# Performance work log

Hardware: AMD Instinct MI355X
Metric: run time of the kernel (lower is better)

Reference implementation:

```python
import jax, jax.numpy as jnp
import numpy as np

EPS_BN = 1e-3  # nn.BatchNorm1d(num_channels, eps=0.001)
B, C, N = 16, 256, 2048
NUM_SA = 4


def _bn(x, g, b, m, v):
    # eval-mode BatchNorm1d over channel dim of [B, C, N]
    return g[:, None] * (x - m[:, None]) * jax.lax.rsqrt(v[:, None] + EPS_BN) + b[:, None]


def _sa_layer(x, qk_w, v_w, v_b, t_w, t_b, g, b, m, var):
    # q_conv and k_conv share weights -> energy = (Wx)^T (Wx)
    q = jnp.einsum('oc,bcn->bon', qk_w, x)              # [B, C//4, N]
    energy = jnp.einsum('bcm,bcn->bmn', q, q)           # [B, N, N]
    attn = jax.nn.softmax(energy, axis=-1)
    # offset-attention: extra column-sum normalization (dim=1)
    attn = attn / (1e-9 + attn.sum(axis=1, keepdims=True))
    xv = jnp.einsum('oc,bcn->bon', v_w, x) + v_b[:, None]   # [B, C, N]
    x_r = jnp.einsum('bcn,bnm->bcm', xv, attn)              # bmm(x_v, attention)
    t = jnp.einsum('oc,bcn->bon', t_w, x - x_r) + t_b[:, None]
    return x + jax.nn.relu(_bn(t, g, b, m, var))


def setup_inputs() -> dict:
    key = jax.random.key(0)
    ks = jax.random.split(key, 24)
    f32 = jnp.float32
    d = {}
    d['x'] = jax.random.normal(ks[0], (B, C, N), dtype=f32)
    d['conv1_w'] = jax.random.normal(ks[1], (C, C), dtype=f32) * 0.05
    d['conv2_w'] = jax.random.normal(ks[2], (C, C), dtype=f32) * 0.05
    for i, nm in enumerate(['bn1', 'bn2']):
        kk = jax.random.split(ks[3 + i], 4)
        d[nm + '_g'] = 1.0 + 0.05 * jax.random.normal(kk[0], (C,), dtype=f32)
        d[nm + '_b'] = 0.05 * jax.random.normal(kk[1], (C,), dtype=f32)
        d[nm + '_m'] = 0.05 * jax.random.normal(kk[2], (C,), dtype=f32)
        d[nm + '_v'] = jax.random.uniform(kk[3], (C,), dtype=f32, minval=0.5, maxval=1.5)
    d['sa_qk_w'] = jax.random.normal(ks[5], (NUM_SA, C // 4, C), dtype=f32) * 0.05
    d['sa_v_w'] = jax.random.normal(ks[6], (NUM_SA, C, C), dtype=f32) * 0.05
    d['sa_v_b'] = jax.random.normal(ks[7], (NUM_SA, C), dtype=f32) * 0.05
    d['sa_t_w'] = jax.random.normal(ks[8], (NUM_SA, C, C), dtype=f32) * 0.05
    d['sa_t_b'] = jax.random.normal(ks[9], (NUM_SA, C), dtype=f32) * 0.05
    d['sa_g'] = 1.0 + 0.05 * jax.random.normal(ks[10], (NUM_SA, C), dtype=f32)
    d['sa_b'] = 0.05 * jax.random.normal(ks[11], (NUM_SA, C), dtype=f32)
    d['sa_m'] = 0.05 * jax.random.normal(ks[12], (NUM_SA, C), dtype=f32)
    d['sa_var'] = jax.random.uniform(ks[13], (NUM_SA, C), dtype=f32, minval=0.5, maxval=1.5)
    d['flag'] = 0  # False -> primary bn branch
    return d


def reference(x, conv1_w, conv2_w, bn1_g, bn1_b, bn1_m, bn1_v,
              bn2_g, bn2_b, bn2_m, bn2_v,
              sa_qk_w, sa_v_w, sa_v_b, sa_t_w, sa_t_b,
              sa_g, sa_b, sa_m, sa_var, flag):
    h = jax.nn.relu(_bn(jnp.einsum('oc,bcn->bon', conv1_w, x), bn1_g, bn1_b, bn1_m, bn1_v))
    h = jax.nn.relu(_bn(jnp.einsum('oc,bcn->bon', conv2_w, h), bn2_g, bn2_b, bn2_m, bn2_v))
    outs = []
    for i in range(NUM_SA):
        h = _sa_layer(h, sa_qk_w[i], sa_v_w[i], sa_v_b[i], sa_t_w[i], sa_t_b[i],
                      sa_g[i], sa_b[i], sa_m[i], sa_var[i])
        outs.append(h)
    return jnp.concatenate(outs, axis=1)  # [B, 4*C, N]
```

## Files before the change

kernel.cpp:

```cpp
#include <hip/hip_runtime.h>
#include <hip/hip_bf16.h>
#include <hip/hip_fp16.h>

static constexpr int Bn = 16;
static constexpr int Cc = 256;
static constexpr int Nn = 2048;
static constexpr int C4 = 64;
static constexpr float LOG2E = 1.4426950408889634f;

typedef _Float16 half_t;
typedef __attribute__((ext_vector_type(8))) _Float16 half8;
typedef __attribute__((ext_vector_type(4))) _Float16 half4;
typedef __attribute__((ext_vector_type(8))) short short8;
typedef __attribute__((ext_vector_type(4))) float float4v;

static constexpr long sNC = (long)Nn * Cc;
static constexpr long sNQ = (long)Nn * C4;

#define DEVI __device__ __forceinline__

DEVI float bf2f(unsigned short u) { return __uint_as_float(((unsigned)u) << 16); }
DEVI unsigned short f2bf(float f) {
    unsigned x = __float_as_uint(f);
    x += 0x7fffu + ((x >> 16) & 1u);
    return (unsigned short)(x >> 16);
}

DEVI void gload16(const void* g, void* l) {
    __builtin_amdgcn_global_load_lds(
        (const __attribute__((address_space(1))) unsigned int*)g,
        (__attribute__((address_space(3))) unsigned int*)l, 16, 0, 0);
}

enum { EPI_RAW = 0, EPI_H = 1, EPI_XV = 2 };

template<int MODE, int BM, int BN, int WI, int WJ, bool BF16OUT>
__global__ __launch_bounds__(WI * WJ * 64)
void mgemm(const half_t* __restrict__ A, long aB,
           const half_t* __restrict__ Bm, long bB,
           void* __restrict__ Yv, long yB, int ldy,
           const float* __restrict__ bias,
           const float* __restrict__ bng, const float* __restrict__ bnb,
           const float* __restrict__ bnm, const float* __restrict__ bnv,
           int K)
{
    constexpr int NW = WI * WJ;
    __shared__ __align__(16) half_t Als[2][BM][32];
    __shared__ __align__(16) half_t Bls[2][BN][32];

    const int tid  = threadIdx.x;
    const int w    = tid >> 6;
    const int lane = tid & 63;
    const int wi   = w % WI;
    const int wj   = w / WI;
    const int quad = lane >> 4, m16 = lane & 15;
    const int lr   = lane >> 2, lc = lane & 3;
    const int b    = blockIdx.z;
    const int j0   = blockIdx.x * BN;
    const int i0   = blockIdx.y * BM;

    const half_t* Ab = A + (size_t)b * aB;
    const half_t* Bb = Bm + (size_t)b * bB;

    float4v acc[4][4];
    #pragma unroll
    for (int i = 0; i < 4; ++i)
        #pragma unroll
        for (int j = 0; j < 4; ++j) acc[i][j] = (float4v)0.f;

    for (int k0 = 0; k0 < K; k0 += 64) {
        #pragma unroll
        for (int s = 0; s < 2; ++s) {
            const int kk = k0 + s * 32 + lc * 8;
            #pragma unroll
            for (int t = 0; t < BM / (16 * NW); ++t) {
                const int row = (t * NW + w) * 16;
                gload16(Ab + (size_t)(i0 + row + lr) * K + kk, &Als[s][row][0]);
            }
            #pragma unroll
            for (int t = 0; t < BN / (16 * NW); ++t) {
                const int row = (t * NW + w) * 16;
                gload16(Bb + (size_t)(j0 + row + lr) * K + kk, &Bls[s][row][0]);
            }
        }
        __syncthreads();
        #pragma unroll
        for (int s = 0; s < 2; ++s) {
            half8 af[4], bf[4];
            #pragma unroll
            for (int t = 0; t < 4; ++t)
                af[t] = *(const half8*)&Als[s][wi * 64 + t * 16 + m16][quad * 8];
            #pragma unroll
            for (int t = 0; t < 4; ++t)
                bf[t] = *(const half8*)&Bls[s][wj * 64 + t * 16 + m16][quad * 8];
            #pragma unroll
            for (int ti = 0; ti < 4; ++ti)
                #pragma unroll
                for (int tj = 0; tj < 4; ++tj)
                    acc[ti][tj] = __builtin_amdgcn_mfma_f32_16x16x32_f16(
                        af[ti], bf[tj], acc[ti][tj], 0, 0, 0);
        }
        __syncthreads();
    }

    #pragma unroll
    for (int ti = 0; ti < 4; ++ti) {
        const int il = i0 + wi * 64 + ti * 16 + quad * 4;
        #pragma unroll
        for (int tj = 0; tj < 4; ++tj) {
            const int jl = j0 + wj * 64 + tj * 16 + m16;
            float4v v = acc[ti][tj];
            if (MODE == EPI_RAW) {
                half4 o;
                #pragma unroll
                for (int r = 0; r < 4; ++r) o[r] = (half_t)v[r];
                *(half4*)((half_t*)Yv + (size_t)b * yB + (size_t)jl * ldy + il) = o;
            } else if (MODE == EPI_H) {
                half4 o;
                #pragma unroll
                for (int r = 0; r < 4; ++r) {
                    const float sc = bng[il + r] * rsqrtf(bnv[il + r] + 1e-3f);
                    const float sh = bnb[il + r] - bnm[il + r] * sc;
                    o[r] = (half_t)fmaxf(fmaf(v[r], sc, sh), 0.f);
                }
                *(half4*)((half_t*)Yv + (size_t)b * yB + (size_t)jl * ldy + il) = o;
            } else {
                const float bj = bias[jl];
                if (BF16OUT) {
                    ushort4 o;
                    o.x = f2bf(v[0] + bj); o.y = f2bf(v[1] + bj);
                    o.z = f2bf(v[2] + bj); o.w = f2bf(v[3] + bj);
                    *(ushort4*)((unsigned short*)Yv + (size_t)b * yB + (size_t)jl * ldy + il) = o;
                } else {
                    half4 o;
                    #pragma unroll
                    for (int r = 0; r < 4; ++r) o[r] = (half_t)(v[r] + bj);
                    *(half4*)((half_t*)Yv + (size_t)b * yB + (size_t)jl * ldy + il) = o;
                }
            }
        }
    }
}

__global__ __launch_bounds__(256)
void estats(const half_t* __restrict__ q, float* __restrict__ Pbuf)
{
    __shared__ __align__(16) half_t sA[128 * 64];
    __shared__ __align__(16) half_t sB[128 * 64];
    __shared__ float red[2][2][4][16][2];
    const int tid = threadIdx.x, w = tid >> 6, lane = tid & 63;
    const int wi = w & 1, wj = w >> 1, quad = lane >> 4, m16 = lane & 15;
    const int b = blockIdx.z, j0 = blockIdx.x * 128, i0 = blockIdx.y * 128;
    const half_t* qb = q + (size_t)b * sNQ;

    #pragma unroll
    for (int t = 0; t < 4; ++t) {
        const int g = w * 256 + t * 64 + lane;
        const int r = g >> 3, c = g & 7;
        const int cs = c ^ (r & 7);
        gload16(qb + (size_t)(i0 + r) * 64 + cs * 8, sA + (w * 256 + t * 64) * 8);
        gload16(qb + (size_t)(j0 + r) * 64 + cs * 8, sB + (w * 256 + t * 64) * 8);
    }
    __syncthreads();

    half8 an[4][2], bm[4][2];
    #pragma unroll
    for (int t = 0; t < 4; ++t)
        #pragma unroll
        for (int ks = 0; ks < 2; ++ks) {
            const int pc = ((ks * 4 + quad) ^ (m16 & 7)) * 8;
            an[t][ks] = *(const half8*)&sA[(wi * 64 + t * 16 + m16) * 64 + pc];
            bm[t][ks] = *(const half8*)&sB[(wj * 64 + t * 16 + m16) * 64 + pc];
        }

    #pragma unroll
    for (int tj = 0; tj < 4; ++tj) {
        float4v e[4];
        #pragma unroll
        for (int ti = 0; ti < 4; ++ti) {
            e[ti] = (float4v)0.f;
            e[ti] = __builtin_amdgcn_mfma_f32_16x16x32_f16(an[ti][0], bm[tj][0], e[ti], 0, 0, 0);
            e[ti] = __builtin_amdgcn_mfma_f32_16x16x32_f16(an[ti][1], bm[tj][1], e[ti], 0, 0, 0);
        }
        float lmax = -1e30f;
        #pragma unroll
        for (int ti = 0; ti < 4; ++ti)
            #pragma unroll
            for (int r = 0; r < 4; ++r) lmax = fmaxf(lmax, e[ti][r]);
        lmax = fmaxf(lmax, __shfl_xor(lmax, 16));
        lmax = fmaxf(lmax, __shfl_xor(lmax, 32));
        float ls = 0.f;
        #pragma unroll
        for (int ti = 0; ti < 4; ++ti)
            #pragma unroll
            for (int r = 0; r < 4; ++r) ls += __expf(e[ti][r] - lmax);
        ls += __shfl_xor(ls, 16);
        ls += __shfl_xor(ls, 32);
        if (quad == 0) { red[wi][wj][tj][m16][0] = lmax; red[wi][wj][tj][m16][1] = ls; }
    }
    __syncthreads();
    if (tid < 128) {
        const int wj2 = tid >> 6, tj2 = (tid >> 4) & 3, mm = tid & 15;
        const float m0 = red[0][wj2][tj2][mm][0], s0 = red[0][wj2][tj2][mm][1];
        const float m1 = red[1][wj2][tj2][mm][0], s1 = red[1][wj2][tj2][mm][1];
        const float M = fmaxf(m0, m1);
        const float S = s0 * __expf(m0 - M) + s1 * __expf(m1 - M);
        const int m = j0 + wj2 * 64 + tj2 * 16 + mm;
        *(float2*)(Pbuf + (((size_t)b * Nn + m) * 16 + blockIdx.y) * 2) = make_float2(M, S);
    }
}

__global__ __launch_bounds__(512)
void flashxr(const half_t* __restrict__ q, const half_t* __restrict__ xv,
             const half_t* __restrict__ h, const float* __restrict__ Pbuf,
             const half_t* __restrict__ tw, const float* __restrict__ tb,
             const float* __restrict__ bng, const float* __restrict__ bnb,
             const float* __restrict__ bnm, const float* __restrict__ bnv,
             float* __restrict__ outL, half_t* __restrict__ hNext)
{
    __shared__ __align__(16) half_t sXV[256 * 64];
    __shared__ __align__(16) half_t sQA[2][64 * 64];
    __shared__ __align__(16) half_t sP[64 * 64];
    __shared__ float sOff[Nn];

    const int tid = threadIdx.x, w = tid >> 6, lane = tid & 63;
    const int quad = lane >> 4, m16 = lane & 15;
    const int wiE = w & 1, wjE = w >> 1;
    const int wi = w & 3, wj = w >> 2;
    const int wjT = w;
    const int f = blockIdx.x;
    const int W = (f & 7) * 64 + (f >> 3);
    const int b = W >> 5, j0 = (W & 31) * 64;
    const half_t* qb  = q + (size_t)b * sNQ;
    const half_t* xvb = xv + (size_t)b * sNC;

    const int sr = tid >> 3, sc = tid & 7;
    const int qsw = (sc ^ (sr & 7)) * 8;

    gload16(qb + (size_t)sr * 64 + qsw, &sQA[0][(size_t)tid * 8]);

    half8 bq[2];
    #pragma unroll
    for (int s = 0; s < 2; ++s)
        bq[s] = *(const half8*)(qb + (size_t)(j0 + wjE * 16 + m16) * 64 + (s * 4 + quad) * 8);

    {
        const float* pB = Pbuf + (size_t)b * Nn * 32;
        for (int i = tid; i < Nn; i += 512) {
            const float4v* p4 = (const float4v*)(pB + (size_t)i * 32);
            float4v v[8];
            #pragma unroll
            for (int t = 0; t < 8; ++t) v[t] = p4[t];
            float M = -1e30f;
            #pragma unroll
            for (int t = 0; t < 8; ++t) { M = fmaxf(M, v[t][0]); M = fmaxf(M, v[t][2]); }
            float S = 0.f;
            #pragma unroll
            for (int t = 0; t < 8; ++t) {
                S += v[t][1] * __expf(v[t][0] - M);
                S += v[t][3] * __expf(v[t][2] - M);
            }
            sOff[i] = fmaf(M, LOG2E, __log2f(S));
        }
    }
    __syncthreads();

    float4v acc[4][2];
    #pragma unroll
    for (int i = 0; i < 4; ++i)
        #pragma unroll
        for (int j = 0; j < 2; ++j) acc[i][j] = (float4v)0.f;
    float csa = 0.f;
    const int mrow = wjE * 16 + m16;

    for (int nc = 0; nc < 32; ++nc) {
        #pragma unroll
        for (int t = 0; t < 4; ++t) {
            const int g = t * 512 + tid;
            const int r = g >> 3, c = g & 7;
            gload16(xvb + (size_t)r * Nn + nc * 64 + ((c ^ (r & 7)) * 8),
                    sXV + (size_t)g * 8);
        }
        if (nc < 31)
            gload16(qb + (size_t)((nc + 1) * 64 + sr) * 64 + qsw,
                    &sQA[(nc + 1) & 1][(size_t)tid * 8]);
        __syncthreads();

        const half_t* qA = &sQA[nc & 1][0];
        const int nbase = nc * 64 + wiE * 32 + quad * 4;
        #pragma unroll
        for (int ti = 0; ti < 2; ++ti) {
            const int nl = wiE * 32 + ti * 16 + m16;
            const half8 an0 = *(const half8*)&qA[(size_t)nl * 64 + ((quad ^ (m16 & 7)) * 8)];
            const half8 an1 = *(const half8*)&qA[(size_t)nl * 64 + (((4 + quad) ^ (m16 & 7)) * 8)];
            float4v e = (float4v)0.f;
            e = __builtin_amdgcn_mfma_f32_16x16x32_f16(an0, bq[0], e, 0, 0, 0);
            e = __builtin_amdgcn_mfma_f32_16x16x32_f16(an1, bq[1], e, 0, 0, 0);
            const float4v o4 = *(const float4v*)&sOff[nbase + ti * 16];
            float c0 = 0.f; ushort4 pk;
            #pragma unroll
            for (int r = 0; r < 4; ++r) {
                const float p = __builtin_amdgcn_exp2f(fmaf(e[r], LOG2E, -o4[r]));
                c0 += p; (&pk.x)[r] = f2bf(p);
            }
            csa += c0;
            const int pc = (wiE * 4 + ti * 2 + (quad >> 1)) ^ (m16 & 7);
            *(ushort4*)&((unsigned short*)sP)[(size_t)mrow * 64 + pc * 8 + (quad & 1) * 4] = pk;
        }
        __syncthreads();

        #pragma unroll
        for (int ks = 0; ks < 2; ++ks) {
            short8 xa[4], pb[2];
            #pragma unroll
            for (int ti = 0; ti < 4; ++ti)
                xa[ti] = *(const short8*)&sXV[(size_t)(wi * 64 + ti * 16 + m16) * 64
                                              + (((ks * 4 + quad) ^ (m16 & 7)) * 8)];
            #pragma unroll
            for (int tj = 0; tj < 2; ++tj)
                pb[tj] = *(const short8*)&sP[(size_t)(wj * 32 + tj * 16 + m16) * 64
                                             + (((ks * 4 + quad) ^ (m16 & 7)) * 8)];
            __builtin_amdgcn_s_setprio(1);
            #pragma unroll
            for (int ti = 0; ti < 4; ++ti)
                #pragma unroll
                for (int tj = 0; tj < 2; ++tj)
                    acc[ti][tj] = __builtin_amdgcn_mfma_f32_16x16x32_bf16(
                        xa[ti], pb[tj], acc[ti][tj], 0, 0, 0);
            __builtin_amdgcn_s_setprio(0);
        }
        __syncthreads();
    }

    csa += __shfl_xor(csa, 16);
    csa += __shfl_xor(csa, 32);
    float* fb = (float*)sP;
    if (lane < 16) fb[wiE * 64 + wjE * 16 + lane] = csa;
    __syncthreads();
    float csr[2];
    #pragma unroll
    for (int tj = 0; tj < 2; ++tj) {
        const int m = wj * 32 + tj * 16 + m16;
        csr[tj] = 1.0f / (1e-9f + fb[m] + fb[64 + m]);
    }

    const half_t* hb = h + (size_t)b * sNC;
    half_t* sD = sXV;
    #pragma unroll
    for (int ti = 0; ti < 4; ++ti) {
        const int cg = wi * 64 + ti * 16 + quad * 4;
        const int cc = (cg >> 3) ^ (m16 & 7);
        const int sub = (quad & 1) * 4;
        #pragma unroll
        for (int tj = 0; tj < 2; ++tj) {
            const int mr = wj * 32 + tj * 16 + m16;
            const int mg = j0 + mr;
            const half4 hv = *(const half4*)&hb[(size_t)mg * Cc + cg];
            half4 o;
            #pragma unroll
            for (int r = 0; r < 4; ++r)
                o[r] = (half_t)((float)hv[r] - acc[ti][tj][r] * csr[tj]);
            *(half4*)&sD[(size_t)mr * 256 + cc * 8 + sub] = o;
        }
    }
    __syncthreads();

    float4v acc2[4][2];
    #pragma unroll
    for (int i = 0; i < 4; ++i)
        #pragma unroll
        for (int j = 0; j < 2; ++j) acc2[i][j] = (float4v)0.f;
    #pragma unroll
    for (int ks = 0; ks < 8; ++ks) {
        half8 af[4], bf[2];
        #pragma unroll
        for (int tm = 0; tm < 4; ++tm)
            af[tm] = *(const half8*)&sD[(size_t)(tm * 16 + m16) * 256
                                        + (((ks * 4 + quad) ^ (m16 & 7)) * 8)];
        #pragma unroll
        for (int tc = 0; tc < 2; ++tc)
            bf[tc] = *(const half8*)&tw[(size_t)(wjT * 32 + tc * 16 + m16) * 256
                                        + ks * 32 + quad * 8];
        #pragma unroll
        for (int tm = 0; tm < 4; ++tm)
            #pragma unroll
            for (int tc = 0; tc < 2; ++tc)
                acc2[tm][tc] = __builtin_amdgcn_mfma_f32_16x16x32_f16(
                    af[tm], bf[tc], acc2[tm][tc], 0, 0, 0);
    }

    const long yB = (long)4 * Cc * Nn;
    float* yb = outL + (size_t)b * yB;
    half_t* hn = hNext ? hNext + (size_t)b * sNC : nullptr;
    #pragma unroll
    for (int tc = 0; tc < 2; ++tc) {
        const int co = wjT * 32 + tc * 16 + m16;
        const float tb2 = tb[co];
        const float sc2 = bng[co] * rsqrtf(bnv[co] + 1e-3f);
        const float sh2 = bnb[co] - bnm[co] * sc2;
        #pragma unroll
        for (int tm = 0; tm < 4; ++tm) {
            const int mg = j0 + tm * 16 + quad * 4;
            float4v o;
            #pragma unroll
            for (int r = 0; r < 4; ++r) {
                const float t2  = acc2[tm][tc][r] + tb2;
                const float rel = fmaxf(fmaf(t2, sc2, sh2), 0.f);
                const float hv  = (float)hb[(size_t)(mg + r) * Cc + co];
                const float ov  = hv + rel;
                o[r] = ov;
                if (hn) hn[(size_t)(mg + r) * Cc + co] = (half_t)ov;
            }
            *(float4v*)&yb[(size_t)co * Nn + mg] = o;
        }
    }
}

__global__ __launch_bounds__(256)
void xpose_cast(const float* __restrict__ x, half_t* __restrict__ xT)
{
    __shared__ half_t tile[32][33];
    const int tx = threadIdx.x & 31, ty = threadIdx.x >> 5;
    const int n0 = blockIdx.x * 32, c0 = blockIdx.y * 32, b = blockIdx.z;
    #pragma unroll
    for (int r = 0; r < 4; ++r)
        tile[ty * 4 + r][tx] =
            (half_t)x[((size_t)b * Cc + c0 + ty * 4 + r) * Nn + n0 + tx];
    __syncthreads();
    #pragma unroll
    for (int r = 0; r < 4; ++r)
        xT[((size_t)b * Nn + n0 + ty * 4 + r) * Cc + c0 + tx] = tile[tx][ty * 4 + r];
}

__global__ __launch_bounds__(256)
void castall(const float* __restrict__ c1, const float* __restrict__ c2,
             const float* __restrict__ qk, const float* __restrict__ vw,
             const float* __restrict__ tw, half_t* __restrict__ dst)
{
    const int i = (blockIdx.x * 256 + threadIdx.x) * 4;
    const float* s; int o;
    if      (i < 65536)  { s = c1; o = 0; }
    else if (i < 131072) { s = c2; o = 65536; }
    else if (i < 196608) { s = qk; o = 131072; }
    else if (i < 458752) { s = vw; o = 196608; }
    else                 { s = tw; o = 458752; }
    const float4v v = *(const float4v*)(s + (i - o));
    half4 out;
    #pragma unroll
    for (int r = 0; r < 4; ++r) out[r] = (half_t)v[r];
    *(half4*)(dst + i) = out;
}

extern "C" void kernel_launch(void* const* d_in, const int* in_sizes, int n_in,
                              void* d_out, int out_size, void* d_ws, size_t ws_size,
                              hipStream_t stream)
{
    const float* x    = (const float*)d_in[0];
    const float* c1w  = (const float*)d_in[1];
    const float* c2w  = (const float*)d_in[2];
    const float* bn1g = (const float*)d_in[3], *bn1b = (const float*)d_in[4];
    const float* bn1m = (const float*)d_in[5], *bn1v = (const float*)d_in[6];
    const float* bn2g = (const float*)d_in[7], *bn2b = (const float*)d_in[8];
    const float* bn2m = (const float*)d_in[9], *bn2v = (const float*)d_in[10];
    const float* qkw  = (const float*)d_in[11];
    const float* vw   = (const float*)d_in[12];
    const float* vb   = (const float*)d_in[13];
    const float* tw   = (const float*)d_in[14];
    const float* tb   = (const float*)d_in[15];
    const float* sag  = (const float*)d_in[16];
    const float* sab  = (const float*)d_in[17];
    const float* sam  = (const float*)d_in[18];
    const float* sav  = (const float*)d_in[19];
    float* out = (float*)d_out;

    char* ws = (char*)d_ws;
    const size_t HSZ = (size_t)Bn * Nn * Cc * 2;
    half_t* xT   = (half_t*)(ws);
    half_t* hA   = (half_t*)(ws + HSZ);
    half_t* hBuf = (half_t*)(ws + 2 * HSZ);
    half_t* q_s  = (half_t*)(ws + 3 * HSZ);
    half_t* xv_s = (half_t*)(ws + 3 * HSZ + (size_t)4194304);
    float*  Pbuf = (float*) (ws + 4 * HSZ + (size_t)4194304);
    half_t* warena = (half_t*)(ws + 4 * HSZ + (size_t)8388608);
    half_t* wc1  = warena;
    half_t* wc2  = wc1 + 65536;
    half_t* wqk  = wc2 + 65536;
    half_t* wv   = wqk + 65536;
    half_t* wt   = wv  + 262144;

    dim3 blk(256);

    castall<<<768, blk, 0, stream>>>(c1w, c2w, qkw, vw, tw, warena);
    xpose_cast<<<dim3(Nn / 32, Cc / 32, Bn), blk, 0, stream>>>(x, xT);

    mgemm<EPI_H, 256, 128, 4, 2, false><<<dim3(16, 1, Bn), dim3(512), 0, stream>>>(
        wc1, 0, xT, sNC, hA, sNC, Cc,
        nullptr, bn1g, bn1b, bn1m, bn1v, Cc);
    mgemm<EPI_H, 256, 128, 4, 2, false><<<dim3(16, 1, Bn), dim3(512), 0, stream>>>(
        wc2, 0, hA, sNC, hBuf, sNC, Cc,
        nullptr, bn2g, bn2b, bn2m, bn2v, Cc);

    half_t* hcur = hBuf;
    half_t* hnxt = hA;
    for (int L = 0; L < 4; ++L) {
        mgemm<EPI_RAW, 64, 256, 1, 4, false><<<dim3(8, 1, Bn), blk, 0, stream>>>(
            wqk + (long)L * C4 * Cc, 0, hcur, sNC, q_s, sNQ, C4,
            nullptr, nullptr, nullptr, nullptr, nullptr, Cc);
        estats<<<dim3(16, 16, Bn), blk, 0, stream>>>(q_s, Pbuf);
        mgemm<EPI_XV, 128, 256, 2, 4, true><<<dim3(1, 16, Bn), dim3(512), 0, stream>>>(
            hcur, sNC, wv + (long)L * Cc * Cc, 0, xv_s, (long)Cc * Nn, Nn,
            vb + L * Cc, nullptr, nullptr, nullptr, nullptr, Cc);
        flashxr<<<dim3(512), dim3(512), 0, stream>>>(
            q_s, xv_s, hcur, Pbuf,
            wt + (long)L * Cc * Cc, tb + L * Cc,
            sag + L * Cc, sab + L * Cc, sam + L * Cc, sav + L * Cc,
            out + (long)L * Cc * Nn, (L < 3) ? hnxt : nullptr);
        half_t* tmp = hcur; hcur = hnxt; hnxt = tmp;
    }
}
```

Measured before the change: 722.8 us.

## Compute full column softmax stats in estats with online merge, drop partial buffer

The estats kernel now has each 512-thread block own 128 columns and stream all 2048 rows of q through double-buffered shared memory. It keeps an online running max and sum and writes the final log2 offset per column directly. This removes the 16-way partial (max, sum) buffer and the reduction flashxr used to do over it, so flashxr only loads the offsets. The cost is a launch of just 256 blocks and a barrier per chunk, which may reduce parallelism and latency hiding.

```diff
diff --git a/kernel.cpp b/kernel.cpp
--- a/kernel.cpp
+++ b/kernel.cpp
@@ -142,77 +142,119 @@
     }
 }
 
-__global__ __launch_bounds__(256)
-void estats(const half_t* __restrict__ q, float* __restrict__ Pbuf)
+__global__ __launch_bounds__(512)
+void estats(const half_t* __restrict__ q, float* __restrict__ off)
 {
-    __shared__ __align__(16) half_t sA[128 * 64];
-    __shared__ __align__(16) half_t sB[128 * 64];
-    __shared__ float red[2][2][4][16][2];
+    __shared__ __align__(16) half_t sQB[128 * 64];
+    __shared__ __align__(16) half_t sQA[2][256 * 64];
+    __shared__ float red[2][2][4][2][16][2];
+
     const int tid = threadIdx.x, w = tid >> 6, lane = tid & 63;
-    const int wi = w & 1, wj = w >> 1, quad = lane >> 4, m16 = lane & 15;
-    const int b = blockIdx.z, j0 = blockIdx.x * 128, i0 = blockIdx.y * 128;
+    const int quad = lane >> 4, m16 = lane & 15;
+    const int wi = w & 1, wj = w >> 1;
+    const int f = blockIdx.x;
+    const int W = (f & 7) * 32 + (f >> 3);
+    const int b = W >> 4, j0 = (W & 15) * 128;
     const half_t* qb = q + (size_t)b * sNQ;
 
     #pragma unroll
+    for (int t = 0; t < 2; ++t) {
+        const int g = t * 512 + tid;
+        const int r = g >> 3, c = g & 7;
+        gload16(qb + (size_t)(j0 + r) * 64 + ((c ^ (r & 7)) * 8), sQB + (size_t)g * 8);
+    }
+    #pragma unroll
     for (int t = 0; t < 4; ++t) {
-        const int g = w * 256 + t * 64 + lane;
+        const int g = t * 512 + tid;
         const int r = g >> 3, c = g & 7;
-        const int cs = c ^ (r & 7);
-        gload16(qb + (size_t)(i0 + r) * 64 + cs * 8, sA + (w * 256 + t * 64) * 8);
-        gload16(qb + (size_t)(j0 + r) * 64 + cs * 8, sB + (w * 256 + t * 64) * 8);
+        gload16(qb + (size_t)r * 64 + ((c ^ (r & 7)) * 8), &sQA[0][(size_t)g * 8]);
     }
     __syncthreads();
 
-    half8 an[4][2], bm[4][2];
-    #pragma unroll
-    for (int t = 0; t < 4; ++t)
-        #pragma unroll
-        for (int ks = 0; ks < 2; ++ks) {
-            const int pc = ((ks * 4 + quad) ^ (m16 & 7)) * 8;
-            an[t][ks] = *(const half8*)&sA[(wi * 64 + t * 16 + m16) * 64 + pc];
-            bm[t][ks] = *(const half8*)&sB[(wj * 64 + t * 16 + m16) * 64 + pc];
-        }
-
-    #pragma unroll
-    for (int tj = 0; tj < 4; ++tj) {
-        float4v e[4];
-        #pragma unroll
-        for (int ti = 0; ti < 4; ++ti) {
-            e[ti] = (float4v)0.f;
-            e[ti] = __builtin_amdgcn_mfma_f32_16x16x32_f16(an[ti][0], bm[tj][0], e[ti], 0, 0, 0);
-            e[ti] = __builtin_amdgcn_mfma_f32_16x16x32_f16(an[ti][1], bm[tj][1], e[ti], 0, 0, 0);
-        }
-        float lmax = -1e30f;
-        #pragma unroll
-        for (int ti = 0; ti < 4; ++ti)
-            #pragma unroll
-            for (int r = 0; r < 4; ++r) lmax = fmaxf(lmax, e[ti][r]);
-        lmax = fmaxf(lmax, __shfl_xor(lmax, 16));
-        lmax = fmaxf(lmax, __shfl_xor(lmax, 32));
-        float ls = 0.f;
-        #pragma unroll
-        for (int ti = 0; ti < 4; ++ti)
-            #pragma unroll
-            for (int r = 0; r < 4; ++r) ls += __expf(e[ti][r] - lmax);
-        ls += __shfl_xor(ls, 16);
-        ls += __shfl_xor(ls, 32);
-        if (quad == 0) { red[wi][wj][tj][m16][0] = lmax; red[wi][wj][tj][m16][1] = ls; }
-    }
-    __syncthreads();
-    if (tid < 128) {
-        const int wj2 = tid >> 6, tj2 = (tid >> 4) & 3, mm = tid & 15;
-        const float m0 = red[0][wj2][tj2][mm][0], s0 = red[0][wj2][tj2][mm][1];
-        const float m1 = red[1][wj2][tj2][mm][0], s1 = red[1][wj2][tj2][mm][1];
-        const float M = fmaxf(m0, m1);
-        const float S = s0 * __expf(m0 - M) + s1 * __expf(m1 - M);
-        const int m = j0 + wj2 * 64 + tj2 * 16 + mm;
-        *(float2*)(Pbuf + (((size_t)b * Nn + m) * 16 + blockIdx.y) * 2) = make_float2(M, S);
+    half8 bq[2][2];
+    #pragma unroll
+    for (int tj = 0; tj < 2; ++tj)
+        #pragma unroll
+        for (int ks = 0; ks < 2; ++ks)
+            bq[tj][ks] = *(const half8*)&sQB[(size_t)(wj * 32 + tj * 16 + m16) * 64
+                                             + (((ks * 4 + quad) ^ (m16 & 7)) * 8)];
+
+    float Mrun[2] = {-1e30f, -1e30f}, Srun[2] = {0.f, 0.f};
+
+    for (int ch = 0; ch < 8; ++ch) {
+        if (ch < 7) {
+            #pragma unroll
+            for (int t = 0; t < 4; ++t) {
+                const int g = t * 512 + tid;
+                const int r = g >> 3, c = g & 7;
+                gload16(qb + (size_t)((ch + 1) * 256 + r) * 64 + ((c ^ (r & 7)) * 8),
+                        &sQA[(ch + 1) & 1][(size_t)g * 8]);
+            }
+        }
+        const half_t* qA = &sQA[ch & 1][0];
+        float Mc[2] = {-1e30f, -1e30f}, Sc[2] = {0.f, 0.f};
+        #pragma unroll
+        for (int ti = 0; ti < 8; ++ti) {
+            const int nl = wi * 128 + ti * 16 + m16;
+            const half8 an0 = *(const half8*)&qA[(size_t)nl * 64 + ((quad ^ (m16 & 7)) * 8)];
+            const half8 an1 = *(const half8*)&qA[(size_t)nl * 64 + (((4 + quad) ^ (m16 & 7)) * 8)];
+            #pragma unroll
+            for (int tj = 0; tj < 2; ++tj) {
+                float4v e = (float4v)0.f;
+                e = __builtin_amdgcn_mfma_f32_16x16x32_f16(an0, bq[tj][0], e, 0, 0, 0);
+                e = __builtin_amdgcn_mfma_f32_16x16x32_f16(an1, bq[tj][1], e, 0, 0, 0);
+                const float tmax = fmaxf(fmaxf(e[0], e[1]), fmaxf(e[2], e[3]));
+                const float nM = fmaxf(Mc[tj], tmax);
+                float s = 0.f;
+                #pragma unroll
+                for (int r = 0; r < 4; ++r) s += __expf(e[r] - nM);
+                Sc[tj] = Sc[tj] * __expf(Mc[tj] - nM) + s;
+                Mc[tj] = nM;
+            }
+        }
+        #pragma unroll
+        for (int tj = 0; tj < 2; ++tj) {
+            #pragma unroll
+            for (int d = 16; d <= 32; d <<= 1) {
+                const float oM = __shfl_xor(Mc[tj], d);
+                const float oS = __shfl_xor(Sc[tj], d);
+                const float nM = fmaxf(Mc[tj], oM);
+                Sc[tj] = Sc[tj] * __expf(Mc[tj] - nM) + oS * __expf(oM - nM);
+                Mc[tj] = nM;
+            }
+        }
+        const int rb = ch & 1;
+        if (quad == 0) {
+            #pragma unroll
+            for (int tj = 0; tj < 2; ++tj) {
+                red[rb][wi][wj][tj][m16][0] = Mc[tj];
+                red[rb][wi][wj][tj][m16][1] = Sc[tj];
+            }
+        }
+        __syncthreads();
+        #pragma unroll
+        for (int tj = 0; tj < 2; ++tj) {
+            const float m0 = red[rb][0][wj][tj][m16][0], s0 = red[rb][0][wj][tj][m16][1];
+            const float m1 = red[rb][1][wj][tj][m16][0], s1 = red[rb][1][wj][tj][m16][1];
+            const float cM = fmaxf(m0, m1);
+            const float cS = s0 * __expf(m0 - cM) + s1 * __expf(m1 - cM);
+            const float nM = fmaxf(Mrun[tj], cM);
+            Srun[tj] = Srun[tj] * __expf(Mrun[tj] - nM) + cS * __expf(cM - nM);
+            Mrun[tj] = nM;
+        }
+    }
+
+    if (wi == 0 && quad == 0) {
+        #pragma unroll
+        for (int tj = 0; tj < 2; ++tj)
+            off[(size_t)b * Nn + j0 + wj * 32 + tj * 16 + m16] =
+                fmaf(Mrun[tj], LOG2E, __log2f(Srun[tj]));
     }
 }
 
 __global__ __launch_bounds__(512)
 void flashxr(const half_t* __restrict__ q, const half_t* __restrict__ xv,
-             const half_t* __restrict__ h, const float* __restrict__ Pbuf,
+             const half_t* __restrict__ h, const float* __restrict__ offp,
              const half_t* __restrict__ tw, const float* __restrict__ tb,
              const float* __restrict__ bng, const float* __restrict__ bnb,
              const float* __restrict__ bnm, const float* __restrict__ bnv,
@@ -238,31 +280,13 @@
     const int qsw = (sc ^ (sr & 7)) * 8;
 
     gload16(qb + (size_t)sr * 64 + qsw, &sQA[0][(size_t)tid * 8]);
+    gload16(offp + (size_t)b * Nn + (size_t)tid * 4, sOff + (size_t)tid * 4);
 
     half8 bq[2];
     #pragma unroll
     for (int s = 0; s < 2; ++s)
         bq[s] = *(const half8*)(qb + (size_t)(j0 + wjE * 16 + m16) * 64 + (s * 4 + quad) * 8);
 
-    {
-        const float* pB = Pbuf + (size_t)b * Nn * 32;
-        for (int i = tid; i < Nn; i += 512) {
-            const float4v* p4 = (const float4v*)(pB + (size_t)i * 32);
-            float4v v[8];
-            #pragma unroll
-            for (int t = 0; t < 8; ++t) v[t] = p4[t];
-            float M = -1e30f;
-            #pragma unroll
-            for (int t = 0; t < 8; ++t) { M = fmaxf(M, v[t][0]); M = fmaxf(M, v[t][2]); }
-            float S = 0.f;
-            #pragma unroll
-            for (int t = 0; t < 8; ++t) {
-                S += v[t][1] * __expf(v[t][0] - M);
-                S += v[t][3] * __expf(v[t][2] - M);
-            }
-            sOff[i] = fmaf(M, LOG2E, __log2f(S));
-        }
-    }
     __syncthreads();
 
     float4v acc[4][2];
@@ -480,7 +504,7 @@
     half_t* hBuf = (half_t*)(ws + 2 * HSZ);
     half_t* q_s  = (half_t*)(ws + 3 * HSZ);
     half_t* xv_s = (half_t*)(ws + 3 * HSZ + (size_t)4194304);
-    float*  Pbuf = (float*) (ws + 4 * HSZ + (size_t)4194304);
+    float*  offp = (float*) (ws + 4 * HSZ + (size_t)4194304);
     half_t* warena = (half_t*)(ws + 4 * HSZ + (size_t)8388608);
     half_t* wc1  = warena;
     half_t* wc2  = wc1 + 65536;
@@ -506,12 +530,12 @@
         mgemm<EPI_RAW, 64, 256, 1, 4, false><<<dim3(8, 1, Bn), blk, 0, stream>>>(
             wqk + (long)L * C4 * Cc, 0, hcur, sNC, q_s, sNQ, C4,
             nullptr, nullptr, nullptr, nullptr, nullptr, Cc);
-        estats<<<dim3(16, 16, Bn), blk, 0, stream>>>(q_s, Pbuf);
+        estats<<<dim3(256), dim3(512), 0, stream>>>(q_s, offp);
         mgemm<EPI_XV, 128, 256, 2, 4, true><<<dim3(1, 16, Bn), dim3(512), 0, stream>>>(
             hcur, sNC, wv + (long)L * Cc * Cc, 0, xv_s, (long)Cc * Nn, Nn,
             vb + L * Cc, nullptr, nullptr, nullptr, nullptr, Cc);
         flashxr<<<dim3(512), dim3(512), 0, stream>>>(
-            q_s, xv_s, hcur, Pbuf,
+            q_s, xv_s, hcur, offp,
             wt + (long)L * Cc * Cc, tb + L * Cc,
             sag + L * Cc, sab + L * Cc, sam + L * Cc, sav + L * Cc,
             out + (long)L * Cc * Nn, (L < 3) ? hnxt : nullptr);
```

Result: faster. 704.4 us (-2.6%).
